# Performance work log

Hardware: AMD Instinct MI355X
Metric: run time of the kernel (lower is better)

Reference implementation:

```python
import jax, jax.numpy as jnp
import numpy as np

N = 50000
E = 600000
D_IN = 128
D_HID = 128
D_OUT = 40
EPS = 1e-5


def glorot(key, shape):
    lim = float(np.sqrt(6.0 / (shape[0] + shape[1])))
    return jax.random.uniform(key, shape, jnp.float32, -lim, lim)


def setup_inputs() -> dict:
    key = jax.random.key(0)
    ks = jax.random.split(key, 8)
    return {
        "node_feat": jax.random.normal(ks[0], (N, D_IN), jnp.float32),
        "edge_src": jax.random.randint(ks[1], (E,), 0, N, jnp.int32),
        "edge_dst": jax.random.randint(ks[2], (E,), 0, N, jnp.int32),
        # input BatchNorm (bn_1)
        "bn0_g": jnp.ones((D_IN,), jnp.float32),
        "bn0_b": jnp.zeros((D_IN,), jnp.float32),
        # conv 1 (in -> hidden) + its BN
        "W1": glorot(ks[3], (D_IN, D_HID)),
        "b1": jnp.zeros((D_HID,), jnp.float32),
        "bn1_g": jnp.ones((D_HID,), jnp.float32),
        "bn1_b": jnp.zeros((D_HID,), jnp.float32),
        # conv 2 (hidden -> hidden) + its BN
        "W2": glorot(ks[4], (D_HID, D_HID)),
        "b2": jnp.zeros((D_HID,), jnp.float32),
        "bn2_g": jnp.ones((D_HID,), jnp.float32),
        "bn2_b": jnp.zeros((D_HID,), jnp.float32),
        # final projection
        "Wf": glorot(ks[5], (D_HID, D_OUT)),
        "bf": jnp.zeros((D_OUT,), jnp.float32),
    }


def batchnorm(x, gamma, beta):
    # BatchNorm1d over nodes (batch-stat / training-mode normalization)
    mu = jnp.mean(x, axis=0)
    var = jnp.mean(jnp.square(x - mu), axis=0)
    return gamma * (x - mu) * jax.lax.rsqrt(var + EPS) + beta


def gcn_conv(x, W, b, src, dst, norm, self_norm):
    # GCNConv: D^{-1/2}(A+I)D^{-1/2} X W + b
    h = x @ W  # [N, d_out]
    agg = jax.ops.segment_sum(h[src] * norm[:, None], dst, num_segments=N)
    agg = agg + h * self_norm[:, None]  # self-loop contribution
    return agg + b


def reference(node_feat, edge_src, edge_dst, bn0_g, bn0_b, W1, b1, bn1_g, bn1_b,
              W2, b2, bn2_g, bn2_b, Wf, bf):
    # degree with self-loops: deg_i = |{e : dst(e)=i}| + 1
    deg = jnp.ones((N,), jnp.float32).at[edge_dst].add(1.0)
    dinv = jax.lax.rsqrt(deg)
    norm = dinv[edge_src] * dinv[edge_dst]  # [E]
    self_norm = dinv * dinv                 # [N]

    x = batchnorm(node_feat, bn0_g, bn0_b)

    x = gcn_conv(x, W1, b1, edge_src, edge_dst, norm, self_norm)
    x = batchnorm(x, bn1_g, bn1_b)
    x = jax.nn.relu(x)  # dropout is identity in eval mode

    x = gcn_conv(x, W2, b2, edge_src, edge_dst, norm, self_norm)
    x = batchnorm(x, bn2_g, bn2_b)
    x = jax.nn.relu(x)

    return x @ Wf + bf  # [N, D_OUT]
```

## Files before the change

### kernel.cpp

```cpp
#include <hip/hip_runtime.h>
#include <cstdint>
#include <cstddef>


#define CS_BLOCKS 512

typedef short s8v __attribute__((ext_vector_type(8)));
typedef float f4v __attribute__((ext_vector_type(4)));

__device__ inline ushort f2bf(float f) {
    uint u = __float_as_uint(f);
    return (ushort)((u + 0x7fffu + ((u >> 16) & 1u)) >> 16);
}
__device__ inline float2 bf2f2(uint u) {
    float2 r;
    r.x = __uint_as_float(u << 16);
    r.y = __uint_as_float(u & 0xffff0000u);
    return r;
}

__global__ __launch_bounds__(256) void k_init(const float* __restrict__ W1,
                                              const float* __restrict__ W2,
                                              ushort* __restrict__ Wswz,
                                              int* __restrict__ cnt, int n) {
    const int bid = blockIdx.x;
    if (bid < 16) {
        const float* W = (bid < 8) ? W1 : W2;
        ushort* out = Wswz + (bid < 8 ? 0 : 16384);
        int t  = (bid & 7) * 256 + threadIdx.x;
        int l  = t & 63;
        int fi = t >> 6;
        int ks = fi & 3, ct = fi >> 2;
        int c  = ct * 16 + (l & 15);
        int k0 = ks * 32 + ((l >> 4) << 3);
        ushort o[8];
        #pragma unroll
        for (int j = 0; j < 8; ++j)
            o[j] = f2bf(W[(size_t)(k0 + j) * 128 + c]);
        ushort4* dst = (ushort4*)(out + (size_t)t * 8);
        dst[0] = make_ushort4(o[0], o[1], o[2], o[3]);
        dst[1] = make_ushort4(o[4], o[5], o[6], o[7]);
    } else {
        const int nv = n >> 2;
        int4* c4 = (int4*)cnt;
        const int4 z = make_int4(0, 0, 0, 0);
        for (int i = (bid - 16) * 256 + threadIdx.x; i < nv; i += 64 * 256)
            c4[i] = z;
        int tail0 = nv << 2;
        int i = tail0 + (bid - 16) * 256 + threadIdx.x;
        if (i < n) cnt[i] = 0;
    }
}

__global__ __launch_bounds__(256) void k_colstats(const float* __restrict__ X,
                                                  int n,
                                                  float* __restrict__ part) {
    __shared__ float ls[8 * 128];
    __shared__ float lq[8 * 128];
    const int c4    = threadIdx.x & 31;
    const int rslot = threadIdx.x >> 5;
    float4 s4 = make_float4(0.f, 0.f, 0.f, 0.f);
    float4 q4 = make_float4(0.f, 0.f, 0.f, 0.f);
    const float4* X4 = (const float4*)X;
    for (int r = blockIdx.x * 8 + rslot; r < n; r += CS_BLOCKS * 8) {
        float4 v = X4[(size_t)r * 32 + c4];
        s4.x += v.x; s4.y += v.y; s4.z += v.z; s4.w += v.w;
        q4.x = fmaf(v.x, v.x, q4.x); q4.y = fmaf(v.y, v.y, q4.y);
        q4.z = fmaf(v.z, v.z, q4.z); q4.w = fmaf(v.w, v.w, q4.w);
    }
    *(float4*)&ls[rslot * 128 + c4 * 4] = s4;
    *(float4*)&lq[rslot * 128 + c4 * 4] = q4;
    __syncthreads();
    float t = 0.f;
    if (threadIdx.x < 128) {
        int c = threadIdx.x;
        #pragma unroll
        for (int k = 0; k < 8; ++k) t += ls[k * 128 + c];
    } else {
        int c = threadIdx.x - 128;
        #pragma unroll
        for (int k = 0; k < 8; ++k) t += lq[k * 128 + c];
    }
    part[blockIdx.x * 256 + threadIdx.x] = t;
}

__global__ __launch_bounds__(256) void k_redA(const float* __restrict__ part,
                                              float* __restrict__ part2,
                                              int nrows) {
    const int c = threadIdx.x;
    const int b = blockIdx.x;
    const int per = (nrows + 63) >> 6;
    const int r0 = b * per;
    const int r1 = min(r0 + per, nrows);
    float t0 = 0.f, t1 = 0.f;
    int r = r0;
    for (; r + 2 <= r1; r += 2) {
        t0 += part[(size_t)r * 256 + c];
        t1 += part[(size_t)(r + 1) * 256 + c];
    }
    if (r < r1) t0 += part[(size_t)r * 256 + c];
    part2[b * 256 + c] = t0 + t1;
}

__global__ __launch_bounds__(1024) void k_bnfinal(const float* __restrict__ part,
                                                  int nrows,
                                                  const float* __restrict__ g,
                                                  const float* __restrict__ be,
                                                  float invn,
                                                  float* __restrict__ a,
                                                  float* __restrict__ b) {
    __shared__ float sh[4][256];
    const int c = threadIdx.x & 255;
    const int q = threadIdx.x >> 8;
    const int per = nrows >> 2;
    float t = 0.f;
    for (int r = q * per; r < q * per + per; r += 4) {
        t += part[(r + 0) * 256 + c] + part[(r + 1) * 256 + c]
           + part[(r + 2) * 256 + c] + part[(r + 3) * 256 + c];
    }
    sh[q][c] = t;
    __syncthreads();
    if (threadIdx.x < 128) {
        int cc = threadIdx.x;
        float su = sh[0][cc] + sh[1][cc] + sh[2][cc] + sh[3][cc];
        float sq = sh[0][cc + 128] + sh[1][cc + 128]
                 + sh[2][cc + 128] + sh[3][cc + 128];
        float mu  = su * invn;
        float var = sq * invn - mu * mu;
        float av  = g[cc] * rsqrtf(var + 1e-5f);
        a[cc] = av;
        b[cc] = be[cc] - mu * av;
    }
}

__global__ __launch_bounds__(256) void k_count(const int* __restrict__ dst, int e,
                                               int* __restrict__ cnt,
                                               int* __restrict__ rank) {
    int i = blockIdx.x * 256 + threadIdx.x;
    if (i < e) rank[i] = atomicAdd(&cnt[dst[i]], 1);
}

__global__ __launch_bounds__(1024) void k_scanA(const int* __restrict__ cnt, int n,
                                                int* __restrict__ rs, int* __restrict__ bsum) {
    __shared__ int tmp[1024];
    int t = threadIdx.x;
    int i = blockIdx.x * 1024 + t;
    int v = (i < n) ? cnt[i] : 0;
    tmp[t] = v;
    __syncthreads();
    for (int off = 1; off < 1024; off <<= 1) {
        int x = (t >= off) ? tmp[t - off] : 0;
        __syncthreads();
        tmp[t] += x;
        __syncthreads();
    }
    if (i < n) rs[i] = tmp[t] - v;
    if (t == 1023) bsum[blockIdx.x] = tmp[t];
}

__global__ __launch_bounds__(256) void k_scanC(int* __restrict__ rs,
                                               const int* __restrict__ bsum,
                                               const int* __restrict__ cnt,
                                               float* __restrict__ dinv,
                                               int n, int e) {
    __shared__ int base;
    int chunk = (int)(blockIdx.x >> 2);
    if (threadIdx.x == 0) {
        int s = 0;
        for (int c = 0; c < chunk; ++c) s += bsum[c];
        base = s;
    }
    __syncthreads();
    int i = blockIdx.x * 256 + threadIdx.x;
    if (i < n) {
        rs[i] += base;
        dinv[i] = rsqrtf((float)(cnt[i] + 1));
    }
    if (blockIdx.x == 0 && threadIdx.x == 0) rs[n] = e;
}

__global__ __launch_bounds__(256) void k_fill(const int* __restrict__ src,
                                              const int* __restrict__ dst, int e,
                                              const int* __restrict__ rs,
                                              const int* __restrict__ rank,
                                              const float* __restrict__ dinv,
                                              int2* __restrict__ ep) {
    int i = blockIdx.x * 256 + threadIdx.x;
    if (i < e) {
        int d = dst[i], s = src[i];
        int p = rs[d] + rank[i];
        float nm = dinv[s] * dinv[d];
        ep[p] = make_int2(s, __float_as_int(nm));
    }
}

__global__ __launch_bounds__(256) void k_gemm_mfma(const float* __restrict__ X,
                                                   const ushort* __restrict__ Wswz,
                                                   const float* __restrict__ av,
                                                   const float* __restrict__ bv,
                                                   int relu,
                                                   ushort* __restrict__ H, int n) {
    __shared__ ushort xb[64 * 128];
    const int tid  = threadIdx.x;
    const int row0 = blockIdx.x * 64;

    for (int i = tid; i < 64 * 32; i += 256) {
        int r = i >> 5, c4 = i & 31;
        int gr = row0 + r;
        float4 v = make_float4(0.f, 0.f, 0.f, 0.f);
        if (gr < n) v = ((const float4*)X)[(size_t)gr * 32 + c4];
        float4 a4 = ((const float4*)av)[c4];
        float4 b4 = ((const float4*)bv)[c4];
        v.x = fmaf(v.x, a4.x, b4.x);
        v.y = fmaf(v.y, a4.y, b4.y);
        v.z = fmaf(v.z, a4.z, b4.z);
        v.w = fmaf(v.w, a4.w, b4.w);
        if (relu) {
            v.x = fmaxf(v.x, 0.f); v.y = fmaxf(v.y, 0.f);
            v.z = fmaxf(v.z, 0.f); v.w = fmaxf(v.w, 0.f);
        }
        ushort4 pk = make_ushort4(f2bf(v.x), f2bf(v.y), f2bf(v.z), f2bf(v.w));
        int off = (r * 256 + c4 * 8) ^ ((r & 7) << 4);
        *(ushort4*)((char*)xb + off) = pk;
    }
    __syncthreads();

    const int wv = tid >> 6;
    const int l  = tid & 63;
    const int arow = wv * 16 + (l & 15);

    s8v afr[4];
    #pragma unroll
    for (int ks = 0; ks < 4; ++ks) {
        int off = (arow * 256 + ks * 64 + ((l >> 4) << 4)) ^ ((arow & 7) << 4);
        afr[ks] = *(const s8v*)((const char*)xb + off);
    }

    const s8v* wf = (const s8v*)Wswz;
    f4v acc[8];
    #pragma unroll
    for (int ct = 0; ct < 8; ++ct) {
        f4v c = {0.f, 0.f, 0.f, 0.f};
        #pragma unroll
        for (int ks = 0; ks < 4; ++ks) {
            s8v bb = wf[(ct * 4 + ks) * 64 + l];
            c = __builtin_amdgcn_mfma_f32_16x16x32_bf16(afr[ks], bb, c, 0, 0, 0);
        }
        acc[ct] = c;
    }

    const int rbase = row0 + wv * 16 + ((l >> 4) << 2);
    const int cidx  = l & 15;
    #pragma unroll
    for (int r = 0; r < 4; ++r) {
        int gr = rbase + r;
        if (gr < n) {
            #pragma unroll
            for (int ct = 0; ct < 8; ++ct)
                H[(size_t)gr * 128 + ct * 16 + cidx] = f2bf(acc[ct][r]);
        }
    }
}

__global__ __launch_bounds__(256) void k_aggregate(const ushort* __restrict__ H,
                                                   const int* __restrict__ rs,
                                                   const int2* __restrict__ ep,
                                                   const float* __restrict__ dinv,
                                                   float* __restrict__ AGG,
                                                   float* __restrict__ part, int n) {
    __shared__ float red[4][128];
    __shared__ float redq[4][128];
    const int wv   = threadIdx.x >> 6;
    const int lane = threadIdx.x & 63;
    const int node = blockIdx.x * 4 + wv;
    float sx = 0.f, sy = 0.f, qx = 0.f, qy = 0.f;

    if (node < n) {
        float sn = dinv[node]; sn *= sn;
        float2 self = bf2f2(((const uint*)(H + (size_t)node * 128))[lane]);
        float2 acc;
        acc.x = self.x * sn; acc.y = self.y * sn;
        int i  = rs[node];
        int i1 = rs[node + 1];
        for (; i + 16 <= i1; i += 16) {
            int2 p[16];
            uint v[16];
            #pragma unroll
            for (int k = 0; k < 16; ++k) p[k] = ep[i + k];
            #pragma unroll
            for (int k = 0; k < 16; ++k)
                v[k] = ((const uint*)(H + (size_t)p[k].x * 128))[lane];
            #pragma unroll
            for (int k = 0; k < 16; ++k) {
                float w = __int_as_float(p[k].y);
                float2 f = bf2f2(v[k]);
                acc.x = fmaf(w, f.x, acc.x);
                acc.y = fmaf(w, f.y, acc.y);
            }
        }
        if (i + 8 <= i1) {
            int2 p[8];
            uint v[8];
            #pragma unroll
            for (int k = 0; k < 8; ++k) p[k] = ep[i + k];
            #pragma unroll
            for (int k = 0; k < 8; ++k)
                v[k] = ((const uint*)(H + (size_t)p[k].x * 128))[lane];
            #pragma unroll
            for (int k = 0; k < 8; ++k) {
                float w = __int_as_float(p[k].y);
                float2 f = bf2f2(v[k]);
                acc.x = fmaf(w, f.x, acc.x);
                acc.y = fmaf(w, f.y, acc.y);
            }
            i += 8;
        }
        if (i + 4 <= i1) {
            int2 p[4];
            uint v[4];
            #pragma unroll
            for (int k = 0; k < 4; ++k) p[k] = ep[i + k];
            #pragma unroll
            for (int k = 0; k < 4; ++k)
                v[k] = ((const uint*)(H + (size_t)p[k].x * 128))[lane];
            #pragma unroll
            for (int k = 0; k < 4; ++k) {
                float w = __int_as_float(p[k].y);
                float2 f = bf2f2(v[k]);
                acc.x = fmaf(w, f.x, acc.x);
                acc.y = fmaf(w, f.y, acc.y);
            }
            i += 4;
        }
        for (; i < i1; ++i) {
            int2 p = ep[i];
            float w = __int_as_float(p.y);
            float2 f = bf2f2(((const uint*)(H + (size_t)p.x * 128))[lane]);
            acc.x = fmaf(w, f.x, acc.x);
            acc.y = fmaf(w, f.y, acc.y);
        }
        ((float2*)(AGG + (size_t)node * 128))[lane] = acc;
        sx = acc.x; sy = acc.y;
        qx = acc.x * acc.x;
        qy = acc.y * acc.y;
    }

    red[wv][2 * lane]      = sx;
    red[wv][2 * lane + 1]  = sy;
    redq[wv][2 * lane]     = qx;
    redq[wv][2 * lane + 1] = qy;
    __syncthreads();
    const int t = threadIdx.x;
    if (t < 128)
        part[(size_t)blockIdx.x * 256 + t] =
            red[0][t] + red[1][t] + red[2][t] + red[3][t];
    else {
        int c = t - 128;
        part[(size_t)blockIdx.x * 256 + t] =
            redq[0][c] + redq[1][c] + redq[2][c] + redq[3][c];
    }
}

__global__ __launch_bounds__(256) void k_gemm_out(const float* __restrict__ X,
                                                  const float* __restrict__ Wf,
                                                  const float* __restrict__ bfv,
                                                  const float* __restrict__ a,
                                                  const float* __restrict__ b,
                                                  float* __restrict__ OUT, int n) {
    __shared__ float xl[32 * 132];
    __shared__ float wt[40 * 132];
    const int tid = threadIdx.x;

    for (int i = tid; i < 128 * 40; i += 256) {
        int c = i / 40;
        int j = i - c * 40;
        wt[j * 132 + c] = Wf[i];
    }
    const int row0 = blockIdx.x * 32;
    for (int i = tid; i < 32 * 32; i += 256) {
        int r = i >> 5, c4 = i & 31;
        int gr = row0 + r;
        float4 v = make_float4(0.f, 0.f, 0.f, 0.f);
        if (gr < n) v = ((const float4*)X)[(size_t)gr * 32 + c4];
        float4 a4 = ((const float4*)a)[c4];
        float4 b4 = ((const float4*)b)[c4];
        v.x = fmaxf(fmaf(v.x, a4.x, b4.x), 0.f);
        v.y = fmaxf(fmaf(v.y, a4.y, b4.y), 0.f);
        v.z = fmaxf(fmaf(v.z, a4.z, b4.z), 0.f);
        v.w = fmaxf(fmaf(v.w, a4.w, b4.w), 0.f);
        *(float4*)&xl[r * 132 + (c4 << 2)] = v;
    }
    __syncthreads();

    const int rg = tid >> 3;
    const int cg = tid & 7;
    const int j0 = cg * 5;
    float acc[5] = {0.f, 0.f, 0.f, 0.f, 0.f};
    for (int c = 0; c < 128; c += 4) {
        float4 xv = *(const float4*)&xl[rg * 132 + c];
        #pragma unroll
        for (int j = 0; j < 5; ++j) {
            float4 wv = *(const float4*)&wt[(j0 + j) * 132 + c];
            acc[j] = fmaf(xv.x, wv.x, acc[j]);
            acc[j] = fmaf(xv.y, wv.y, acc[j]);
            acc[j] = fmaf(xv.z, wv.z, acc[j]);
            acc[j] = fmaf(xv.w, wv.w, acc[j]);
        }
    }
    int gr = row0 + rg;
    if (gr < n) {
        #pragma unroll
        for (int j = 0; j < 5; ++j)
            OUT[(size_t)gr * 40 + j0 + j] = acc[j] + bfv[j0 + j];
    }
}

extern "C" void kernel_launch(void* const* d_in, const int* in_sizes, int n_in,
                              void* d_out, int out_size, void* d_ws, size_t ws_size,
                              hipStream_t stream) {
    const float* X0      = (const float*)d_in[0];
    const int*   edgesrc = (const int*)d_in[1];
    const int*   edgedst = (const int*)d_in[2];
    const float* bn0g = (const float*)d_in[3];
    const float* bn0b = (const float*)d_in[4];
    const float* W1   = (const float*)d_in[5];
    const float* bn1g = (const float*)d_in[7];
    const float* bn1b = (const float*)d_in[8];
    const float* W2   = (const float*)d_in[9];
    const float* bn2g = (const float*)d_in[11];
    const float* bn2b = (const float*)d_in[12];
    const float* Wf   = (const float*)d_in[13];
    const float* bfv  = (const float*)d_in[14];

    const int n = in_sizes[0] / 128;
    const int e = in_sizes[1];
    float* OUT = (float*)d_out;

    const int aggBlocks = (n + 3) / 4;

    ushort* H    = (ushort*)d_ws;
    float*  AGG  = (float*)(H + (size_t)n * 128);
    float*  dinv = AGG + (size_t)n * 128;
    int2*   ep   = (int2*)(dinv + n);
    ushort* Wswz = (ushort*)(ep + e);
    int*    cnt  = (int*)(Wswz + 2 * 16384);
    int*    rs   = cnt + n;
    int*    rank = rs + n + 1;
    int*    bsum = rank + e;
    float*  part = (float*)(bsum + 64);
    float* part2 = part + (size_t)aggBlocks * 256;
    float* a0 = part2 + 64 * 256;       float* b0 = a0 + 128;
    float* a1 = b0 + 128;               float* b1 = a1 + 128;
    float* a2 = b1 + 128;               float* b2 = a2 + 128;

    const float invn = 1.f / (float)n;
    const int nb = (n + 1023) / 1024;

    k_init<<<80, 256, 0, stream>>>(W1, W2, Wswz, cnt, n);

    k_count<<<(e + 255) / 256, 256, 0, stream>>>(edgedst, e, cnt, rank);
    k_scanA<<<nb, 1024, 0, stream>>>(cnt, n, rs, bsum);
    k_scanC<<<(n + 255) / 256, 256, 0, stream>>>(rs, bsum, cnt, dinv, n, e);
    k_fill<<<(e + 255) / 256, 256, 0, stream>>>(edgesrc, edgedst, e, rs, rank,
                                                dinv, ep);

    const int gemmBlocks = (n + 63) / 64;

    k_colstats<<<CS_BLOCKS, 256, 0, stream>>>(X0, n, part);
    k_bnfinal<<<1, 1024, 0, stream>>>(part, CS_BLOCKS, bn0g, bn0b, invn, a0, b0);
    k_gemm_mfma<<<gemmBlocks, 256, 0, stream>>>(X0, Wswz, a0, b0, 0, H, n);
    k_aggregate<<<aggBlocks, 256, 0, stream>>>(H, rs, ep, dinv, AGG, part, n);

    k_redA<<<64, 256, 0, stream>>>(part, part2, aggBlocks);
    k_bnfinal<<<1, 1024, 0, stream>>>(part2, 64, bn1g, bn1b, invn, a1, b1);
    k_gemm_mfma<<<gemmBlocks, 256, 0, stream>>>(AGG, Wswz + 16384, a1, b1, 1, H, n);
    k_aggregate<<<aggBlocks, 256, 0, stream>>>(H, rs, ep, dinv, AGG, part, n);

    k_redA<<<64, 256, 0, stream>>>(part, part2, aggBlocks);
    k_bnfinal<<<1, 1024, 0, stream>>>(part2, 64, bn2g, bn2b, invn, a2, b2);
    k_gemm_out<<<(n + 31) / 32, 256, 0, stream>>>(AGG, Wf, bfv, a2, b2, OUT, n);
}
```

Before: 251.5 us.

## Merge colstats into init prolog and split aggregate edges across half-waves

The input column-statistics kernel is folded into the weight-swizzle and counter-zero init kernel, so one launch does all three jobs with block ranges picking the role. The aggregation kernel now has each half-wave handle alternate edges with 8-byte loads covering 4 columns per lane. The two halves are combined by a cross-lane shuffle before the store and the stats write. This aims to cut one launch and double the number of edge gathers in flight per wave, at the cost of shuffle work and idle half-waves on odd tails.

Result: faster. 244.5 us (-2.8%).

```diff
diff --git a/kernel.cpp b/kernel.cpp
--- a/kernel.cpp
+++ b/kernel.cpp
@@ -19,15 +19,46 @@
     return r;
 }
 
-__global__ __launch_bounds__(256) void k_init(const float* __restrict__ W1,
-                                              const float* __restrict__ W2,
-                                              ushort* __restrict__ Wswz,
-                                              int* __restrict__ cnt, int n) {
+__global__ __launch_bounds__(256) void k_prolog(const float* __restrict__ X,
+                                                int n, float* __restrict__ part,
+                                                const float* __restrict__ W1,
+                                                const float* __restrict__ W2,
+                                                ushort* __restrict__ Wswz,
+                                                int* __restrict__ cnt) {
     const int bid = blockIdx.x;
-    if (bid < 16) {
-        const float* W = (bid < 8) ? W1 : W2;
-        ushort* out = Wswz + (bid < 8 ? 0 : 16384);
-        int t  = (bid & 7) * 256 + threadIdx.x;
+    if (bid < CS_BLOCKS) {
+        __shared__ float ls[8 * 128];
+        __shared__ float lq[8 * 128];
+        const int c4    = threadIdx.x & 31;
+        const int rslot = threadIdx.x >> 5;
+        float4 s4 = make_float4(0.f, 0.f, 0.f, 0.f);
+        float4 q4 = make_float4(0.f, 0.f, 0.f, 0.f);
+        const float4* X4 = (const float4*)X;
+        for (int r = bid * 8 + rslot; r < n; r += CS_BLOCKS * 8) {
+            float4 v = X4[(size_t)r * 32 + c4];
+            s4.x += v.x; s4.y += v.y; s4.z += v.z; s4.w += v.w;
+            q4.x = fmaf(v.x, v.x, q4.x); q4.y = fmaf(v.y, v.y, q4.y);
+            q4.z = fmaf(v.z, v.z, q4.z); q4.w = fmaf(v.w, v.w, q4.w);
+        }
+        *(float4*)&ls[rslot * 128 + c4 * 4] = s4;
+        *(float4*)&lq[rslot * 128 + c4 * 4] = q4;
+        __syncthreads();
+        float t = 0.f;
+        if (threadIdx.x < 128) {
+            int c = threadIdx.x;
+            #pragma unroll
+            for (int k = 0; k < 8; ++k) t += ls[k * 128 + c];
+        } else {
+            int c = threadIdx.x - 128;
+            #pragma unroll
+            for (int k = 0; k < 8; ++k) t += lq[k * 128 + c];
+        }
+        part[bid * 256 + threadIdx.x] = t;
+    } else if (bid < CS_BLOCKS + 16) {
+        const int wb = bid - CS_BLOCKS;
+        const float* W = (wb < 8) ? W1 : W2;
+        ushort* out = Wswz + (wb < 8 ? 0 : 16384);
+        int t  = (wb & 7) * 256 + threadIdx.x;
         int l  = t & 63;
         int fi = t >> 6;
         int ks = fi & 3, ct = fi >> 2;
@@ -41,47 +72,15 @@
         dst[0] = make_ushort4(o[0], o[1], o[2], o[3]);
         dst[1] = make_ushort4(o[4], o[5], o[6], o[7]);
     } else {
+        const int zb = bid - CS_BLOCKS - 16;
         const int nv = n >> 2;
-        int4* c4 = (int4*)cnt;
+        int4* c4p = (int4*)cnt;
         const int4 z = make_int4(0, 0, 0, 0);
-        for (int i = (bid - 16) * 256 + threadIdx.x; i < nv; i += 64 * 256)
-            c4[i] = z;
-        int tail0 = nv << 2;
-        int i = tail0 + (bid - 16) * 256 + threadIdx.x;
+        for (int i = zb * 256 + threadIdx.x; i < nv; i += 64 * 256)
+            c4p[i] = z;
+        int i = (nv << 2) + zb * 256 + threadIdx.x;
         if (i < n) cnt[i] = 0;
     }
-}
-
-__global__ __launch_bounds__(256) void k_colstats(const float* __restrict__ X,
-                                                  int n,
-                                                  float* __restrict__ part) {
-    __shared__ float ls[8 * 128];
-    __shared__ float lq[8 * 128];
-    const int c4    = threadIdx.x & 31;
-    const int rslot = threadIdx.x >> 5;
-    float4 s4 = make_float4(0.f, 0.f, 0.f, 0.f);
-    float4 q4 = make_float4(0.f, 0.f, 0.f, 0.f);
-    const float4* X4 = (const float4*)X;
-    for (int r = blockIdx.x * 8 + rslot; r < n; r += CS_BLOCKS * 8) {
-        float4 v = X4[(size_t)r * 32 + c4];
-        s4.x += v.x; s4.y += v.y; s4.z += v.z; s4.w += v.w;
-        q4.x = fmaf(v.x, v.x, q4.x); q4.y = fmaf(v.y, v.y, q4.y);
-        q4.z = fmaf(v.z, v.z, q4.z); q4.w = fmaf(v.w, v.w, q4.w);
-    }
-    *(float4*)&ls[rslot * 128 + c4 * 4] = s4;
-    *(float4*)&lq[rslot * 128 + c4 * 4] = q4;
-    __syncthreads();
-    float t = 0.f;
-    if (threadIdx.x < 128) {
-        int c = threadIdx.x;
-        #pragma unroll
-        for (int k = 0; k < 8; ++k) t += ls[k * 128 + c];
-    } else {
-        int c = threadIdx.x - 128;
-        #pragma unroll
-        for (int k = 0; k < 8; ++k) t += lq[k * 128 + c];
-    }
-    part[blockIdx.x * 256 + threadIdx.x] = t;
 }
 
 __global__ __launch_bounds__(256) void k_redA(const float* __restrict__ part,
@@ -262,6 +261,27 @@
     }
 }
 
+template<int NP>
+__device__ inline void pair_batch(const ushort* __restrict__ H,
+                                  const int2* __restrict__ ep,
+                                  int i, int half, int sl,
+                                  float& a0, float& a1, float& a2, float& a3) {
+    int2 p[NP]; uint2 v[NP];
+    #pragma unroll
+    for (int k = 0; k < NP; ++k) p[k] = ep[i + 2 * k + half];
+    #pragma unroll
+    for (int k = 0; k < NP; ++k)
+        v[k] = ((const uint2*)(H + (size_t)p[k].x * 128))[sl];
+    #pragma unroll
+    for (int k = 0; k < NP; ++k) {
+        float w = __int_as_float(p[k].y);
+        float2 f0 = bf2f2(v[k].x);
+        float2 f1 = bf2f2(v[k].y);
+        a0 = fmaf(w, f0.x, a0); a1 = fmaf(w, f0.y, a1);
+        a2 = fmaf(w, f1.x, a2); a3 = fmaf(w, f1.y, a3);
+    }
+}
+
 __global__ __launch_bounds__(256) void k_aggregate(const ushort* __restrict__ H,
                                                    const int* __restrict__ rs,
                                                    const int2* __restrict__ ep,
@@ -272,83 +292,47 @@
     __shared__ float redq[4][128];
     const int wv   = threadIdx.x >> 6;
     const int lane = threadIdx.x & 63;
+    const int half = lane >> 5;
+    const int sl   = lane & 31;
     const int node = blockIdx.x * 4 + wv;
-    float sx = 0.f, sy = 0.f, qx = 0.f, qy = 0.f;
+    float a0 = 0.f, a1 = 0.f, a2 = 0.f, a3 = 0.f;
 
     if (node < n) {
-        float sn = dinv[node]; sn *= sn;
-        float2 self = bf2f2(((const uint*)(H + (size_t)node * 128))[lane]);
-        float2 acc;
-        acc.x = self.x * sn; acc.y = self.y * sn;
+        if (half == 0) {
+            float sn = dinv[node]; sn *= sn;
+            uint2 sv = ((const uint2*)(H + (size_t)node * 128))[sl];
+            float2 f0 = bf2f2(sv.x), f1 = bf2f2(sv.y);
+            a0 = sn * f0.x; a1 = sn * f0.y;
+            a2 = sn * f1.x; a3 = sn * f1.y;
+        }
         int i  = rs[node];
         int i1 = rs[node + 1];
-        for (; i + 16 <= i1; i += 16) {
-            int2 p[16];
-            uint v[16];
-            #pragma unroll
-            for (int k = 0; k < 16; ++k) p[k] = ep[i + k];
-            #pragma unroll
-            for (int k = 0; k < 16; ++k)
-                v[k] = ((const uint*)(H + (size_t)p[k].x * 128))[lane];
-            #pragma unroll
-            for (int k = 0; k < 16; ++k) {
-                float w = __int_as_float(p[k].y);
-                float2 f = bf2f2(v[k]);
-                acc.x = fmaf(w, f.x, acc.x);
-                acc.y = fmaf(w, f.y, acc.y);
-            }
-        }
-        if (i + 8 <= i1) {
-            int2 p[8];
-            uint v[8];
-            #pragma unroll
-            for (int k = 0; k < 8; ++k) p[k] = ep[i + k];
-            #pragma unroll
-            for (int k = 0; k < 8; ++k)
-                v[k] = ((const uint*)(H + (size_t)p[k].x * 128))[lane];
-            #pragma unroll
-            for (int k = 0; k < 8; ++k) {
-                float w = __int_as_float(p[k].y);
-                float2 f = bf2f2(v[k]);
-                acc.x = fmaf(w, f.x, acc.x);
-                acc.y = fmaf(w, f.y, acc.y);
-            }
-            i += 8;
-        }
-        if (i + 4 <= i1) {
-            int2 p[4];
-            uint v[4];
-            #pragma unroll
-            for (int k = 0; k < 4; ++k) p[k] = ep[i + k];
-            #pragma unroll
-            for (int k = 0; k < 4; ++k)
-                v[k] = ((const uint*)(H + (size_t)p[k].x * 128))[lane];
-            #pragma unroll
-            for (int k = 0; k < 4; ++k) {
-                float w = __int_as_float(p[k].y);
-                float2 f = bf2f2(v[k]);
-                acc.x = fmaf(w, f.x, acc.x);
-                acc.y = fmaf(w, f.y, acc.y);
-            }
-            i += 4;
-        }
-        for (; i < i1; ++i) {
+        for (; i + 16 <= i1; i += 16) pair_batch<8>(H, ep, i, half, sl, a0, a1, a2, a3);
+        if (i + 8 <= i1) { pair_batch<4>(H, ep, i, half, sl, a0, a1, a2, a3); i += 8; }
+        if (i + 4 <= i1) { pair_batch<2>(H, ep, i, half, sl, a0, a1, a2, a3); i += 4; }
+        if (i + 2 <= i1) { pair_batch<1>(H, ep, i, half, sl, a0, a1, a2, a3); i += 2; }
+        if (i < i1) {
             int2 p = ep[i];
-            float w = __int_as_float(p.y);
-            float2 f = bf2f2(((const uint*)(H + (size_t)p.x * 128))[lane]);
-            acc.x = fmaf(w, f.x, acc.x);
-            acc.y = fmaf(w, f.y, acc.y);
-        }
-        ((float2*)(AGG + (size_t)node * 128))[lane] = acc;
-        sx = acc.x; sy = acc.y;
-        qx = acc.x * acc.x;
-        qy = acc.y * acc.y;
-    }
-
-    red[wv][2 * lane]      = sx;
-    red[wv][2 * lane + 1]  = sy;
-    redq[wv][2 * lane]     = qx;
-    redq[wv][2 * lane + 1] = qy;
+            float w = (half == 0) ? __int_as_float(p.y) : 0.f;
+            uint2 v = ((const uint2*)(H + (size_t)p.x * 128))[sl];
+            float2 f0 = bf2f2(v.x), f1 = bf2f2(v.y);
+            a0 = fmaf(w, f0.x, a0); a1 = fmaf(w, f0.y, a1);
+            a2 = fmaf(w, f1.x, a2); a3 = fmaf(w, f1.y, a3);
+        }
+        a0 += __shfl_xor(a0, 32);
+        a1 += __shfl_xor(a1, 32);
+        a2 += __shfl_xor(a2, 32);
+        a3 += __shfl_xor(a3, 32);
+        if (half == 0)
+            ((float4*)(AGG + (size_t)node * 128))[sl] =
+                make_float4(a0, a1, a2, a3);
+    }
+
+    if (half == 0) {
+        *(float4*)&red[wv][4 * sl]  = make_float4(a0, a1, a2, a3);
+        *(float4*)&redq[wv][4 * sl] = make_float4(a0 * a0, a1 * a1,
+                                                  a2 * a2, a3 * a3);
+    }
     __syncthreads();
     const int t = threadIdx.x;
     if (t < 128)
@@ -456,7 +440,8 @@
     const float invn = 1.f / (float)n;
     const int nb = (n + 1023) / 1024;
 
-    k_init<<<80, 256, 0, stream>>>(W1, W2, Wswz, cnt, n);
+    k_prolog<<<CS_BLOCKS + 16 + 64, 256, 0, stream>>>(X0, n, part, W1, W2,
+                                                      Wswz, cnt);
 
     k_count<<<(e + 255) / 256, 256, 0, stream>>>(edgedst, e, cnt, rank);
     k_scanA<<<nb, 1024, 0, stream>>>(cnt, n, rs, bsum);
@@ -466,7 +451,6 @@
 
     const int gemmBlocks = (n + 63) / 64;
 
-    k_colstats<<<CS_BLOCKS, 256, 0, stream>>>(X0, n, part);
     k_bnfinal<<<1, 1024, 0, stream>>>(part, CS_BLOCKS, bn0g, bn0b, invn, a0, b0);
     k_gemm_mfma<<<gemmBlocks, 256, 0, stream>>>(X0, Wswz, a0, b0, 0, H, n);
     k_aggregate<<<aggBlocks, 256, 0, stream>>>(H, rs, ep, dinv, AGG, part, n);
```
